# Kernel optimization log

Measured on AMD Instinct MI355X. Metric: run time of the kernel, lower is better.

Reference implementation:

```python
import jax, jax.numpy as jnp
import numpy as np

B, MEM_LEN, DEC_LEN = 8, 512, 32
MEM_H, DEC_H, H = 512, 512, 1024


def setup_inputs() -> dict:
    key = jax.random.key(0)
    ks = jax.random.split(key, 12)
    mem = jax.random.normal(ks[0], (B, MEM_LEN, MEM_H), jnp.float32)
    dec_hid = jax.random.normal(ks[1], (B, DEC_LEN, DEC_H), jnp.float32)
    mem_mask = jax.random.bernoulli(ks[2], 0.1, (B, MEM_LEN))
    dec_mask = jax.random.bernoulli(ks[3], 0.1, (B, DEC_LEN))
    dup_mask = jax.random.bernoulli(ks[4], 0.05, (B, DEC_LEN, MEM_LEN + 1))
    dup_mask = dup_mask.at[:, :, 0].set(False)  # keep terminate slot valid so no all--inf rows
    terminate_state = jax.random.normal(ks[5], (1, MEM_H), jnp.float32) * 0.05
    W_mem = jax.random.normal(ks[6], (H, MEM_H), jnp.float32) * 0.02
    b_mem = jnp.zeros((H,), jnp.float32)
    W_dec = jax.random.normal(ks[7], (H, DEC_H), jnp.float32) * 0.02
    b_dec = jnp.zeros((H,), jnp.float32)
    w_score = jax.random.normal(ks[8], (H,), jnp.float32) * 0.02
    b_score = jnp.zeros((), jnp.float32)
    return {"mem": mem, "dec_hid": dec_hid, "mem_mask": mem_mask, "dec_mask": dec_mask,
            "dup_mask": dup_mask, "terminate_state": terminate_state,
            "W_mem": W_mem, "b_mem": b_mem, "W_dec": W_dec, "b_dec": b_dec,
            "w_score": w_score, "b_score": b_score}


def reference(mem, dec_hid, mem_mask, dec_mask, dup_mask, terminate_state,
              W_mem, b_mem, W_dec, b_dec, w_score, b_score):
    b = mem.shape[0]
    neg_inf = jnp.float32(-jnp.inf)
    # prepend learned terminate state to memory; its mask slot is always valid
    term = jnp.broadcast_to(terminate_state[None], (b, 1, terminate_state.shape[-1]))
    mem_full = jnp.concatenate([term, mem], axis=1)                      # [B, M+1, MEM_H]
    mem_mask_full = jnp.concatenate(
        [jnp.zeros((b, 1), dtype=mem_mask.dtype), mem_mask], axis=1)     # [B, M+1]
    # project once, then broadcast-add (equivalent to Linear on expanded tensors)
    pm = jnp.einsum('bmk,hk->bmh', mem_full, W_mem) + b_mem              # [B, M+1, H]
    pd = jnp.einsum('bdk,hk->bdh', dec_hid, W_dec) + b_dec               # [B, D, H]
    h = jnp.tanh(pm[:, None, :, :] + pd[:, :, None, :])                  # [B, D, M+1, H]
    score = jnp.einsum('bdmh,h->bdm', h, w_score) + b_score              # [B, D, M+1]
    score = jnp.where(mem_mask_full[:, None, :], neg_inf, score)
    # dup_mask rows where dec step is padding are cleared (dup_mask[dec_mask,:]=0)
    dup = jnp.where(dec_mask[:, :, None], False, dup_mask)
    score = jnp.where(dup, neg_inf, score)
    return jax.nn.log_softmax(score, axis=-1)
```

## Files before the change

### kernel.cpp

```cpp
#include <hip/hip_runtime.h>
#include <hip/hip_bf16.h>
#include <math.h>

#define B 8
#define MEM_LEN 512
#define DEC_LEN 32
#define HDIM 1024
#define M1 513
#define PM_ROWS (B * M1)
#define AROWS 4224

#define NEG_BIG (-1e30f)
#define C2F 2.885390081777927f

#if __has_builtin(__builtin_amdgcn_exp2f)
#define EXP2(x) __builtin_amdgcn_exp2f(x)
#else
#define EXP2(x) exp2f(x)
#endif
#define RCP(x) __builtin_amdgcn_rcpf(x)
#define SCHED_FENCE() __builtin_amdgcn_sched_barrier(0)

typedef __bf16 bfv8 __attribute__((ext_vector_type(8)));
typedef float  f4   __attribute__((ext_vector_type(4)));
typedef float  f8   __attribute__((ext_vector_type(8)));

#define N_MF  (AROWS * 512 / 8)
#define N_DEC (256 * 512 / 8)
#define N_W   (1024 * 512 / 8)
#define N_CVT (N_MF + N_DEC + 2 * N_W)

__global__ __launch_bounds__(256) void convert_all(
        const float* __restrict__ mem, const float* __restrict__ term,
        const float* __restrict__ dec_hid,
        const float* __restrict__ W_mem, const float* __restrict__ W_dec,
        __bf16* __restrict__ mfb, __bf16* __restrict__ decb,
        __bf16* __restrict__ wmb, __bf16* __restrict__ wdb) {
    int idx = blockIdx.x * 256 + threadIdx.x;
    float4 v0 = make_float4(0.f, 0.f, 0.f, 0.f), v1 = v0;
    float scale = 1.f;
    __bf16* dst;
    if (idx < N_MF) {
        int row = idx >> 6;
        int c8  = idx & 63;
        dst = mfb + (size_t)idx * 8;
        if (row < PM_ROWS) {
            int b = row / M1, m = row - b * M1;
            const float* src = (m == 0) ? (term + c8 * 8)
                                        : (mem + ((size_t)(b * MEM_LEN + m - 1)) * 512 + c8 * 8);
            v0 = ((const float4*)src)[0];
            v1 = ((const float4*)src)[1];
        }
    } else if (idx < N_MF + N_DEC) {
        int j = idx - N_MF;
        dst = decb + (size_t)j * 8;
        v0 = ((const float4*)dec_hid)[j * 2];
        v1 = ((const float4*)dec_hid)[j * 2 + 1];
    } else if (idx < N_MF + N_DEC + N_W) {
        int j = idx - N_MF - N_DEC;
        dst = wmb + (size_t)j * 8;
        v0 = ((const float4*)W_mem)[j * 2];
        v1 = ((const float4*)W_mem)[j * 2 + 1];
        scale = C2F;
    } else {
        int j = idx - N_MF - N_DEC - N_W;
        dst = wdb + (size_t)j * 8;
        v0 = ((const float4*)W_dec)[j * 2];
        v1 = ((const float4*)W_dec)[j * 2 + 1];
        scale = C2F;
    }
    bfv8 o;
    o[0] = (__bf16)(v0.x * scale); o[1] = (__bf16)(v0.y * scale);
    o[2] = (__bf16)(v0.z * scale); o[3] = (__bf16)(v0.w * scale);
    o[4] = (__bf16)(v1.x * scale); o[5] = (__bf16)(v1.y * scale);
    o[6] = (__bf16)(v1.z * scale); o[7] = (__bf16)(v1.w * scale);
    *(bfv8*)dst = o;
}

__global__ __launch_bounds__(256, 4) void gemm_ls(
        const __bf16* __restrict__ mfb, const __bf16* __restrict__ decb,
        const __bf16* __restrict__ wmb, const __bf16* __restrict__ wdb,
        const float* __restrict__ b_mem, const float* __restrict__ b_dec,
        __bf16* __restrict__ pmb, __bf16* __restrict__ pdb) {
    __shared__ __align__(16) __bf16 Als[2][64 * 64];
    __shared__ __align__(16) __bf16 Bls[2][64 * 64];

    int orig = blockIdx.x;
    int wg   = (orig & 7) * 140 + (orig >> 3);
    int bx   = wg >> 4;
    int by   = wg & 15;

    bool isMem = bx < 66;
    const __bf16* A  = isMem ? mfb : decb;
    const __bf16* Wb = isMem ? wmb : wdb;
    const float* bsel = isMem ? b_mem : b_dec;
    __bf16* Cout      = isMem ? pmb : pdb;
    int row0 = isMem ? bx * 64 : (bx - 66) * 64;
    int n0b  = by * 64;

    int t = threadIdx.x;
    int r0 = t >> 3,          g0 = t & 7;
    int r1 = (t + 256) >> 3,  g1 = t & 7;
    int ds0 = r0 * 128 + ((g0 ^ (r0 & 7)) << 4);
    int ds1 = r1 * 128 + ((g1 ^ (r1 & 7)) << 4);
    const __bf16* aSrc0 = A  + (size_t)(row0 + r0) * 512 + g0 * 8;
    const __bf16* aSrc1 = A  + (size_t)(row0 + r1) * 512 + g1 * 8;
    const __bf16* bSrc0 = Wb + (size_t)(n0b + r0) * 512 + g0 * 8;
    const __bf16* bSrc1 = Wb + (size_t)(n0b + r1) * 512 + g1 * 8;

    int w = t >> 6, l = t & 63;
    int m0w = (w >> 1) * 32, n0w = (w & 1) * 32;
    int lr = l & 15, lq = l >> 4;

    f4 acc[2][2] = {};

    {
        bfv8 a0 = *(const bfv8*)(aSrc0);
        bfv8 a1 = *(const bfv8*)(aSrc1);
        bfv8 b0 = *(const bfv8*)(bSrc0);
        bfv8 b1 = *(const bfv8*)(bSrc1);
        *(bfv8*)((char*)&Als[0][0] + ds0) = a0;
        *(bfv8*)((char*)&Als[0][0] + ds1) = a1;
        *(bfv8*)((char*)&Bls[0][0] + ds0) = b0;
        *(bfv8*)((char*)&Bls[0][0] + ds1) = b1;
    }
    __syncthreads();

    #pragma unroll
    for (int kt = 0; kt < 8; ++kt) {
        const int cur = kt & 1;
        bfv8 na0, na1, nb0, nb1;
        if (kt < 7) {
            const int kn = (kt + 1) * 64;
            na0 = *(const bfv8*)(aSrc0 + kn);
            na1 = *(const bfv8*)(aSrc1 + kn);
            nb0 = *(const bfv8*)(bSrc0 + kn);
            nb1 = *(const bfv8*)(bSrc1 + kn);
        }
        SCHED_FENCE();
        bfv8 aF[2][2], bF[2][2];
        #pragma unroll
        for (int kk = 0; kk < 2; ++kk) {
            int g = kk * 4 + lq;
            #pragma unroll
            for (int i = 0; i < 2; ++i) {
                int rA = m0w + i * 16 + lr;
                aF[kk][i] = *(const bfv8*)((char*)&Als[cur][0] + rA * 128 + ((g ^ (rA & 7)) << 4));
                int rB = n0w + i * 16 + lr;
                bF[kk][i] = *(const bfv8*)((char*)&Bls[cur][0] + rB * 128 + ((g ^ (rB & 7)) << 4));
            }
        }
        #pragma unroll
        for (int kk = 0; kk < 2; ++kk) {
            acc[0][0] = __builtin_amdgcn_mfma_f32_16x16x32_bf16(aF[kk][0], bF[kk][0], acc[0][0], 0, 0, 0);
            acc[0][1] = __builtin_amdgcn_mfma_f32_16x16x32_bf16(aF[kk][0], bF[kk][1], acc[0][1], 0, 0, 0);
            acc[1][0] = __builtin_amdgcn_mfma_f32_16x16x32_bf16(aF[kk][1], bF[kk][0], acc[1][0], 0, 0, 0);
            acc[1][1] = __builtin_amdgcn_mfma_f32_16x16x32_bf16(aF[kk][1], bF[kk][1], acc[1][1], 0, 0, 0);
        }
        if (kt < 7) {
            const int nxt = cur ^ 1;
            *(bfv8*)((char*)&Als[nxt][0] + ds0) = na0;
            *(bfv8*)((char*)&Als[nxt][0] + ds1) = na1;
            *(bfv8*)((char*)&Bls[nxt][0] + ds0) = nb0;
            *(bfv8*)((char*)&Bls[nxt][0] + ds1) = nb1;
        }
        __syncthreads();
    }

    int crow = lq * 4;
    int ccol = lr;
    #pragma unroll
    for (int j = 0; j < 2; ++j) {
        int col = n0b + n0w + j * 16 + ccol;
        float bv = bsel[col] * C2F;
        #pragma unroll
        for (int i = 0; i < 2; ++i) {
            #pragma unroll
            for (int r = 0; r < 4; ++r) {
                int row = row0 + m0w + i * 16 + crow + r;
                Cout[(size_t)row * HDIM + col] = (__bf16)EXP2(acc[i][j][r] + bv);
            }
        }
    }
}

__global__ __launch_bounds__(256, 4) void score6(
        const __bf16* __restrict__ pm, const __bf16* __restrict__ pdb,
        const float* __restrict__ w_score,
        const unsigned char* __restrict__ mem_mask,
        const unsigned char* __restrict__ dec_mask,
        const unsigned char* __restrict__ dup_mask,
        float* __restrict__ sc) {
    __shared__ __bf16 pdl[4][HDIM];
    int bid = blockIdx.x;
    int b    = bid & 7;
    int rest = bid >> 3;
    int dg   = rest & 7;
    int mc   = rest >> 3;
    int t = threadIdx.x, w = t >> 6, l = t & 63;
    int bd0 = b * DEC_LEN + dg * 4;

    {
        int d  = t >> 6;
        int h0 = (t & 63) * 16;
        const bfv8* src = (const bfv8*)(pdb + (size_t)(bd0 + d) * HDIM + h0);
        bfv8* dst = (bfv8*)&pdl[d][h0];
        dst[0] = src[0];
        dst[1] = src[1];
    }

    f8 w22[2];
    float sumw_l = 0.f;
    #pragma unroll
    for (int half = 0; half < 2; ++half) {
        f8 wv = *(const f8*)(w_score + half * 512 + l * 8);
        #pragma unroll
        for (int j = 0; j < 8; ++j) {
            sumw_l += wv[j];
            w22[half][j] = wv[j] * 2.f;
        }
    }
    #pragma unroll
    for (int off = 32; off; off >>= 1) sumw_l += __shfl_xor(sumw_l, off, 64);
    float sumw_all = sumw_l;

    bool dm[4];
    #pragma unroll
    for (int d = 0; d < 4; ++d) dm[d] = dec_mask[bd0 + d] != 0;
    const unsigned char* dup0 = dup_mask + (size_t)bd0 * M1;

    __syncthreads();

    int mbase = mc * 32 + w * 8;
    for (int i = 0; i < 8; ++i) {
        int m = mbase + i;
        if (m >= M1) break;
        bool memm = (m > 0) && (mem_mask[b * MEM_LEN + m - 1] != 0);
        if (memm) {
            if (l == 0) {
                #pragma unroll
                for (int d = 0; d < 4; ++d)
                    sc[(size_t)(bd0 + d) * M1 + m] = NEG_BIG;
            }
            continue;
        }
        const __bf16* pmr = pm + ((size_t)(b * M1 + m)) * HDIM + l * 8;
        bfv8 p0 = *(const bfv8*)(pmr);
        bfv8 p1 = *(const bfv8*)(pmr + 512);
        float ac[4][2] = {};
        #pragma unroll
        for (int d = 0; d < 4; ++d) {
            bfv8 q0 = *(const bfv8*)&pdl[d][l * 8];
            bfv8 q1 = *(const bfv8*)&pdl[d][512 + l * 8];
            #pragma unroll
            for (int j = 0; j < 8; ++j) {
                float e0 = (float)p0[j] * (float)q0[j];
                ac[d][0] = fmaf(w22[0][j], RCP(e0 + 1.f), ac[d][0]);
                float e1 = (float)p1[j] * (float)q1[j];
                ac[d][1] = fmaf(w22[1][j], RCP(e1 + 1.f), ac[d][1]);
            }
        }
        float a0 = ac[0][0] + ac[0][1];
        float a1 = ac[1][0] + ac[1][1];
        float a2 = ac[2][0] + ac[2][1];
        float a3 = ac[3][0] + ac[3][1];
        #pragma unroll
        for (int off = 32; off; off >>= 1) {
            a0 += __shfl_xor(a0, off, 64);
            a1 += __shfl_xor(a1, off, 64);
            a2 += __shfl_xor(a2, off, 64);
            a3 += __shfl_xor(a3, off, 64);
        }
        float s[4];
        s[0] = sumw_all - a0;
        s[1] = sumw_all - a1;
        s[2] = sumw_all - a2;
        s[3] = sumw_all - a3;
        #pragma unroll
        for (int d = 0; d < 4; ++d) {
            bool kill = (!dm[d] && dup0[(size_t)d * M1 + m]);
            s[d] = kill ? NEG_BIG : s[d];
        }
        if (l == 0) {
            #pragma unroll
            for (int d = 0; d < 4; ++d)
                sc[(size_t)(bd0 + d) * M1 + m] = s[d];
        }
    }
}

__global__ __launch_bounds__(512) void softmax_k(const float* __restrict__ sc,
                                                 float* __restrict__ out) {
    __shared__ float red[512];
    int bd = blockIdx.x, t = threadIdx.x;
    const float* row = sc + (size_t)bd * M1;
    float v = row[t];
    float v512 = row[512];
    float lm = (t == 0) ? fmaxf(v, v512) : v;
    red[t] = lm;
    __syncthreads();
    for (int s = 256; s > 0; s >>= 1) {
        if (t < s) red[t] = fmaxf(red[t], red[t + s]);
        __syncthreads();
    }
    float mx = red[0];
    __syncthreads();
    float le = __expf(v - mx);
    if (t == 0) le += __expf(v512 - mx);
    red[t] = le;
    __syncthreads();
    for (int s = 256; s > 0; s >>= 1) {
        if (t < s) red[t] += red[t + s];
        __syncthreads();
    }
    float lse = mx + __logf(red[0]);
    float* orow = out + (size_t)bd * M1;
    orow[t] = v - lse;
    if (t == 0) orow[512] = v512 - lse;
}

extern "C" void kernel_launch(void* const* d_in, const int* in_sizes, int n_in,
                              void* d_out, int out_size, void* d_ws, size_t ws_size,
                              hipStream_t stream) {
    const float* mem      = (const float*)d_in[0];
    const float* dec_hid  = (const float*)d_in[1];
    const unsigned char* mem_mask = (const unsigned char*)d_in[2];
    const unsigned char* dec_mask = (const unsigned char*)d_in[3];
    const unsigned char* dup_mask = (const unsigned char*)d_in[4];
    const float* term     = (const float*)d_in[5];
    const float* W_mem    = (const float*)d_in[6];
    const float* b_mem    = (const float*)d_in[7];
    const float* W_dec    = (const float*)d_in[8];
    const float* b_dec    = (const float*)d_in[9];
    const float* w_score  = (const float*)d_in[10];

    float* out = (float*)d_out;
    char* ws = (char*)d_ws;
    __bf16* mfb  = (__bf16*)ws;
    __bf16* decb = mfb + (size_t)AROWS * 512;
    __bf16* wmb  = decb + (size_t)256 * 512;
    __bf16* wdb  = wmb + (size_t)1024 * 512;
    __bf16* pmb  = wdb + (size_t)1024 * 512;
    __bf16* pdb  = pmb + (size_t)AROWS * HDIM;
    float*  sc   = (float*)(pdb + (size_t)256 * HDIM);

    convert_all<<<N_CVT / 256, 256, 0, stream>>>(mem, term, dec_hid, W_mem, W_dec,
                                                 mfb, decb, wmb, wdb);
    gemm_ls<<<1120, 256, 0, stream>>>(mfb, decb, wmb, wdb, b_mem, b_dec, pmb, pdb);
    score6<<<8 * 8 * 17, 256, 0, stream>>>(pmb, pdb, w_score,
                                           mem_mask, dec_mask, dup_mask, sc);
    softmax_k<<<B * DEC_LEN, 512, 0, stream>>>(sc, out);
}
```

Measured before the change: 52.70 us.

## Fuse fp32-to-bf16 conversion into GEMM loads and keep decoder projection in fp32

Removes the separate convert kernel: the GEMM now reads fp32 mem/term/dec_hid/weights directly, converts to bf16 while staging into LDS, and handles the terminate-row concat and padding rows inline. The decoder projection output is stored as fp32 and staged in LDS as fp32 in the score kernel, which also pre-converts pm values to float once per row. This saves a launch and an intermediate bf16 round trip, but doubles global load bytes per GEMM tile, since weights are re-read as fp32 by every tile, and doubles the score kernel's LDS footprint.

Result: slower. 125.3 us (+137.7%).

```diff
diff --git a/kernel.cpp b/kernel.cpp
--- a/kernel.cpp
+++ b/kernel.cpp
@@ -25,63 +25,21 @@
 typedef float  f4   __attribute__((ext_vector_type(4)));
 typedef float  f8   __attribute__((ext_vector_type(8)));
 
-#define N_MF  (AROWS * 512 / 8)
-#define N_DEC (256 * 512 / 8)
-#define N_W   (1024 * 512 / 8)
-#define N_CVT (N_MF + N_DEC + 2 * N_W)
-
-__global__ __launch_bounds__(256) void convert_all(
+__device__ __forceinline__ bfv8 pack8s(float4 x, float4 y, float s) {
+    bfv8 o;
+    o[0] = (__bf16)(x.x * s); o[1] = (__bf16)(x.y * s);
+    o[2] = (__bf16)(x.z * s); o[3] = (__bf16)(x.w * s);
+    o[4] = (__bf16)(y.x * s); o[5] = (__bf16)(y.y * s);
+    o[6] = (__bf16)(y.z * s); o[7] = (__bf16)(y.w * s);
+    return o;
+}
+
+__global__ __launch_bounds__(256, 4) void gemm_f(
         const float* __restrict__ mem, const float* __restrict__ term,
         const float* __restrict__ dec_hid,
         const float* __restrict__ W_mem, const float* __restrict__ W_dec,
-        __bf16* __restrict__ mfb, __bf16* __restrict__ decb,
-        __bf16* __restrict__ wmb, __bf16* __restrict__ wdb) {
-    int idx = blockIdx.x * 256 + threadIdx.x;
-    float4 v0 = make_float4(0.f, 0.f, 0.f, 0.f), v1 = v0;
-    float scale = 1.f;
-    __bf16* dst;
-    if (idx < N_MF) {
-        int row = idx >> 6;
-        int c8  = idx & 63;
-        dst = mfb + (size_t)idx * 8;
-        if (row < PM_ROWS) {
-            int b = row / M1, m = row - b * M1;
-            const float* src = (m == 0) ? (term + c8 * 8)
-                                        : (mem + ((size_t)(b * MEM_LEN + m - 1)) * 512 + c8 * 8);
-            v0 = ((const float4*)src)[0];
-            v1 = ((const float4*)src)[1];
-        }
-    } else if (idx < N_MF + N_DEC) {
-        int j = idx - N_MF;
-        dst = decb + (size_t)j * 8;
-        v0 = ((const float4*)dec_hid)[j * 2];
-        v1 = ((const float4*)dec_hid)[j * 2 + 1];
-    } else if (idx < N_MF + N_DEC + N_W) {
-        int j = idx - N_MF - N_DEC;
-        dst = wmb + (size_t)j * 8;
-        v0 = ((const float4*)W_mem)[j * 2];
-        v1 = ((const float4*)W_mem)[j * 2 + 1];
-        scale = C2F;
-    } else {
-        int j = idx - N_MF - N_DEC - N_W;
-        dst = wdb + (size_t)j * 8;
-        v0 = ((const float4*)W_dec)[j * 2];
-        v1 = ((const float4*)W_dec)[j * 2 + 1];
-        scale = C2F;
-    }
-    bfv8 o;
-    o[0] = (__bf16)(v0.x * scale); o[1] = (__bf16)(v0.y * scale);
-    o[2] = (__bf16)(v0.z * scale); o[3] = (__bf16)(v0.w * scale);
-    o[4] = (__bf16)(v1.x * scale); o[5] = (__bf16)(v1.y * scale);
-    o[6] = (__bf16)(v1.z * scale); o[7] = (__bf16)(v1.w * scale);
-    *(bfv8*)dst = o;
-}
-
-__global__ __launch_bounds__(256, 4) void gemm_ls(
-        const __bf16* __restrict__ mfb, const __bf16* __restrict__ decb,
-        const __bf16* __restrict__ wmb, const __bf16* __restrict__ wdb,
         const float* __restrict__ b_mem, const float* __restrict__ b_dec,
-        __bf16* __restrict__ pmb, __bf16* __restrict__ pdb) {
+        __bf16* __restrict__ pmb, float* __restrict__ pdf) {
     __shared__ __align__(16) __bf16 Als[2][64 * 64];
     __shared__ __align__(16) __bf16 Bls[2][64 * 64];
 
@@ -91,22 +49,38 @@
     int by   = wg & 15;
 
     bool isMem = bx < 66;
-    const __bf16* A  = isMem ? mfb : decb;
-    const __bf16* Wb = isMem ? wmb : wdb;
+    const float* Wsel = isMem ? W_mem : W_dec;
     const float* bsel = isMem ? b_mem : b_dec;
-    __bf16* Cout      = isMem ? pmb : pdb;
     int row0 = isMem ? bx * 64 : (bx - 66) * 64;
     int n0b  = by * 64;
 
     int t = threadIdx.x;
-    int r0 = t >> 3,          g0 = t & 7;
-    int r1 = (t + 256) >> 3,  g1 = t & 7;
+    int r0 = t >> 3, g0 = t & 7;
+    int r1 = r0 + 32;
     int ds0 = r0 * 128 + ((g0 ^ (r0 & 7)) << 4);
-    int ds1 = r1 * 128 + ((g1 ^ (r1 & 7)) << 4);
-    const __bf16* aSrc0 = A  + (size_t)(row0 + r0) * 512 + g0 * 8;
-    const __bf16* aSrc1 = A  + (size_t)(row0 + r1) * 512 + g1 * 8;
-    const __bf16* bSrc0 = Wb + (size_t)(n0b + r0) * 512 + g0 * 8;
-    const __bf16* bSrc1 = Wb + (size_t)(n0b + r1) * 512 + g1 * 8;
+    int ds1 = r1 * 128 + ((g0 ^ (r1 & 7)) << 4);
+
+    const float* aS0;
+    const float* aS1;
+    if (isMem) {
+        int grow = row0 + r0;
+        if (grow < PM_ROWS) {
+            int bb = grow / M1, mm = grow - bb * M1;
+            aS0 = (mm == 0) ? term : mem + ((size_t)(bb * MEM_LEN + mm - 1)) * 512;
+        } else aS0 = nullptr;
+        grow = row0 + r1;
+        if (grow < PM_ROWS) {
+            int bb = grow / M1, mm = grow - bb * M1;
+            aS1 = (mm == 0) ? term : mem + ((size_t)(bb * MEM_LEN + mm - 1)) * 512;
+        } else aS1 = nullptr;
+    } else {
+        aS0 = dec_hid + (size_t)(row0 + r0) * 512;
+        aS1 = dec_hid + (size_t)(row0 + r1) * 512;
+    }
+    const float* wS0 = Wsel + (size_t)(n0b + r0) * 512;
+    const float* wS1 = Wsel + (size_t)(n0b + r1) * 512;
+    const float4 Z4 = make_float4(0.f, 0.f, 0.f, 0.f);
+    int co = g0 * 8;
 
     int w = t >> 6, l = t & 63;
     int m0w = (w >> 1) * 32, n0w = (w & 1) * 32;
@@ -115,27 +89,35 @@
     f4 acc[2][2] = {};
 
     {
-        bfv8 a0 = *(const bfv8*)(aSrc0);
-        bfv8 a1 = *(const bfv8*)(aSrc1);
-        bfv8 b0 = *(const bfv8*)(bSrc0);
-        bfv8 b1 = *(const bfv8*)(bSrc1);
-        *(bfv8*)((char*)&Als[0][0] + ds0) = a0;
-        *(bfv8*)((char*)&Als[0][0] + ds1) = a1;
-        *(bfv8*)((char*)&Bls[0][0] + ds0) = b0;
-        *(bfv8*)((char*)&Bls[0][0] + ds1) = b1;
+        float4 ax0 = aS0 ? *(const float4*)(aS0 + co)     : Z4;
+        float4 ax1 = aS0 ? *(const float4*)(aS0 + co + 4) : Z4;
+        float4 ay0 = aS1 ? *(const float4*)(aS1 + co)     : Z4;
+        float4 ay1 = aS1 ? *(const float4*)(aS1 + co + 4) : Z4;
+        float4 bx0 = *(const float4*)(wS0 + co);
+        float4 bx1 = *(const float4*)(wS0 + co + 4);
+        float4 by0 = *(const float4*)(wS1 + co);
+        float4 by1 = *(const float4*)(wS1 + co + 4);
+        *(bfv8*)((char*)&Als[0][0] + ds0) = pack8s(ax0, ax1, 1.f);
+        *(bfv8*)((char*)&Als[0][0] + ds1) = pack8s(ay0, ay1, 1.f);
+        *(bfv8*)((char*)&Bls[0][0] + ds0) = pack8s(bx0, bx1, C2F);
+        *(bfv8*)((char*)&Bls[0][0] + ds1) = pack8s(by0, by1, C2F);
     }
     __syncthreads();
 
     #pragma unroll
     for (int kt = 0; kt < 8; ++kt) {
         const int cur = kt & 1;
-        bfv8 na0, na1, nb0, nb1;
+        float4 ax0, ax1, ay0, ay1, bx0, bx1, by0, by1;
         if (kt < 7) {
-            const int kn = (kt + 1) * 64;
-            na0 = *(const bfv8*)(aSrc0 + kn);
-            na1 = *(const bfv8*)(aSrc1 + kn);
-            nb0 = *(const bfv8*)(bSrc0 + kn);
-            nb1 = *(const bfv8*)(bSrc1 + kn);
+            const int kn = (kt + 1) * 64 + co;
+            ax0 = aS0 ? *(const float4*)(aS0 + kn)     : Z4;
+            ax1 = aS0 ? *(const float4*)(aS0 + kn + 4) : Z4;
+            ay0 = aS1 ? *(const float4*)(aS1 + kn)     : Z4;
+            ay1 = aS1 ? *(const float4*)(aS1 + kn + 4) : Z4;
+            bx0 = *(const float4*)(wS0 + kn);
+            bx1 = *(const float4*)(wS0 + kn + 4);
+            by0 = *(const float4*)(wS1 + kn);
+            by1 = *(const float4*)(wS1 + kn + 4);
         }
         SCHED_FENCE();
         bfv8 aF[2][2], bF[2][2];
@@ -159,10 +141,10 @@
         }
         if (kt < 7) {
             const int nxt = cur ^ 1;
-            *(bfv8*)((char*)&Als[nxt][0] + ds0) = na0;
-            *(bfv8*)((char*)&Als[nxt][0] + ds1) = na1;
-            *(bfv8*)((char*)&Bls[nxt][0] + ds0) = nb0;
-            *(bfv8*)((char*)&Bls[nxt][0] + ds1) = nb1;
+            *(bfv8*)((char*)&Als[nxt][0] + ds0) = pack8s(ax0, ax1, 1.f);
+            *(bfv8*)((char*)&Als[nxt][0] + ds1) = pack8s(ay0, ay1, 1.f);
+            *(bfv8*)((char*)&Bls[nxt][0] + ds0) = pack8s(bx0, bx1, C2F);
+            *(bfv8*)((char*)&Bls[nxt][0] + ds1) = pack8s(by0, by1, C2F);
         }
         __syncthreads();
     }
@@ -178,20 +160,22 @@
             #pragma unroll
             for (int r = 0; r < 4; ++r) {
                 int row = row0 + m0w + i * 16 + crow + r;
-                Cout[(size_t)row * HDIM + col] = (__bf16)EXP2(acc[i][j][r] + bv);
+                float e = EXP2(acc[i][j][r] + bv);
+                if (isMem) pmb[(size_t)row * HDIM + col] = (__bf16)e;
+                else       pdf[(size_t)row * HDIM + col] = e;
             }
         }
     }
 }
 
-__global__ __launch_bounds__(256, 4) void score6(
-        const __bf16* __restrict__ pm, const __bf16* __restrict__ pdb,
+__global__ __launch_bounds__(256, 4) void score7(
+        const __bf16* __restrict__ pm, const float* __restrict__ pdf,
         const float* __restrict__ w_score,
         const unsigned char* __restrict__ mem_mask,
         const unsigned char* __restrict__ dec_mask,
         const unsigned char* __restrict__ dup_mask,
         float* __restrict__ sc) {
-    __shared__ __bf16 pdl[4][HDIM];
+    __shared__ float pdl[4][HDIM];
     int bid = blockIdx.x;
     int b    = bid & 7;
     int rest = bid >> 3;
@@ -203,10 +187,9 @@
     {
         int d  = t >> 6;
         int h0 = (t & 63) * 16;
-        const bfv8* src = (const bfv8*)(pdb + (size_t)(bd0 + d) * HDIM + h0);
-        bfv8* dst = (bfv8*)&pdl[d][h0];
-        dst[0] = src[0];
-        dst[1] = src[1];
+        const f4* src = (const f4*)(pdf + (size_t)(bd0 + d) * HDIM + h0);
+        f4* dst = (f4*)&pdl[d][h0];
+        dst[0] = src[0]; dst[1] = src[1]; dst[2] = src[2]; dst[3] = src[3];
     }
 
     f8 w22[2];
@@ -247,17 +230,26 @@
         const __bf16* pmr = pm + ((size_t)(b * M1 + m)) * HDIM + l * 8;
         bfv8 p0 = *(const bfv8*)(pmr);
         bfv8 p1 = *(const bfv8*)(pmr + 512);
+        f8 pf0, pf1;
+        #pragma unroll
+        for (int j = 0; j < 8; ++j) { pf0[j] = (float)p0[j]; pf1[j] = (float)p1[j]; }
         float ac[4][2] = {};
         #pragma unroll
         for (int d = 0; d < 4; ++d) {
-            bfv8 q0 = *(const bfv8*)&pdl[d][l * 8];
-            bfv8 q1 = *(const bfv8*)&pdl[d][512 + l * 8];
+            f4 q0a = *(const f4*)&pdl[d][l * 8];
+            f4 q0b = *(const f4*)&pdl[d][l * 8 + 4];
+            f4 q1a = *(const f4*)&pdl[d][512 + l * 8];
+            f4 q1b = *(const f4*)&pdl[d][512 + l * 8 + 4];
             #pragma unroll
-            for (int j = 0; j < 8; ++j) {
-                float e0 = (float)p0[j] * (float)q0[j];
+            for (int j = 0; j < 4; ++j) {
+                float e0 = pf0[j] * q0a[j];
                 ac[d][0] = fmaf(w22[0][j], RCP(e0 + 1.f), ac[d][0]);
-                float e1 = (float)p1[j] * (float)q1[j];
-                ac[d][1] = fmaf(w22[1][j], RCP(e1 + 1.f), ac[d][1]);
+                float e1 = pf0[j + 4] * q0b[j];
+                ac[d][0] = fmaf(w22[0][j + 4], RCP(e1 + 1.f), ac[d][0]);
+                float e2 = pf1[j] * q1a[j];
+                ac[d][1] = fmaf(w22[1][j], RCP(e2 + 1.f), ac[d][1]);
+                float e3 = pf1[j + 4] * q1b[j];
+                ac[d][1] = fmaf(w22[1][j + 4], RCP(e3 + 1.f), ac[d][1]);
             }
         }
         float a0 = ac[0][0] + ac[0][1];
@@ -336,18 +328,13 @@
 
     float* out = (float*)d_out;
     char* ws = (char*)d_ws;
-    __bf16* mfb  = (__bf16*)ws;
-    __bf16* decb = mfb + (size_t)AROWS * 512;
-    __bf16* wmb  = decb + (size_t)256 * 512;
-    __bf16* wdb  = wmb + (size_t)1024 * 512;
-    __bf16* pmb  = wdb + (size_t)1024 * 512;
-    __bf16* pdb  = pmb + (size_t)AROWS * HDIM;
-    float*  sc   = (float*)(pdb + (size_t)256 * HDIM);
-
-    convert_all<<<N_CVT / 256, 256, 0, stream>>>(mem, term, dec_hid, W_mem, W_dec,
-                                                 mfb, decb, wmb, wdb);
-    gemm_ls<<<1120, 256, 0, stream>>>(mfb, decb, wmb, wdb, b_mem, b_dec, pmb, pdb);
-    score6<<<8 * 8 * 17, 256, 0, stream>>>(pmb, pdb, w_score,
+    __bf16* pmb = (__bf16*)ws;
+    float*  pdf = (float*)(pmb + (size_t)AROWS * HDIM);
+    float*  sc  = pdf + (size_t)256 * HDIM;
+
+    gemm_f<<<1120, 256, 0, stream>>>(mem, term, dec_hid, W_mem, W_dec,
+                                     b_mem, b_dec, pmb, pdf);
+    score7<<<8 * 8 * 17, 256, 0, stream>>>(pmb, pdf, w_score,
                                            mem_mask, dec_mask, dup_mask, sc);
     softmax_k<<<B * DEC_LEN, 512, 0, stream>>>(sc, out);
 }
```
